# Kernel optimization log

Hardware: AMD Instinct MI355X
Metric: run time of the kernel (lower is better)

Reference implementation:

```python
import jax, jax.numpy as jnp
import numpy as np

N = 4_000_000
F = 8   # EXPERIMENTS['full'] feature count
H = 16  # hidden width of both MLPs
NBINS = 28


def _lin_init(k, i, o):
    return jax.random.normal(k, (i, o), jnp.float32) * (1.0 / np.sqrt(i))


def setup_inputs() -> dict:
    key = jax.random.key(0)
    ks = jax.random.split(key, 16)
    inp = {
        "x_feat": jax.random.normal(ks[0], (N, F), jnp.float32),
        # mh MLP params
        "mh_W1": _lin_init(ks[1], F, H), "mh_b1": jnp.zeros((H,), jnp.float32),
        "mh_W2": _lin_init(ks[2], H, H), "mh_b2": jnp.zeros((H,), jnp.float32),
        "mh_W3": _lin_init(ks[3], H, 1), "mh_b3": jnp.zeros((1,), jnp.float32),
        # mh_less MLP params (input dim 1 = Size)
        "ml_W1": _lin_init(ks[4], 1, H), "ml_b1": jnp.zeros((H,), jnp.float32),
        "ml_W2": _lin_init(ks[5], H, H), "ml_b2": jnp.zeros((H,), jnp.float32),
        "ml_W3": _lin_init(ks[6], H, 1), "ml_b3": jnp.zeros((1,), jnp.float32),
    }
    # deletion sizes in 1..40 (some > 28 exercise the skip branch)
    del_lens = jax.random.randint(ks[7], (N,), 1, 41, jnp.int32)
    eq = jax.random.bernoulli(ks[8], 0.3, (N,))
    alt = jax.random.randint(ks[9], (N,), 1, 41, jnp.int32)
    inp["del_lens"] = del_lens
    inp["mh_len"] = jnp.where(eq, del_lens, alt).astype(jnp.int32)
    return inp


def _mlp(x, W1, b1, W2, b2, W3, b3):
    h = jax.nn.sigmoid(x @ W1 + b1)
    h = jax.nn.sigmoid(h @ W2 + b2)
    return h @ W3 + b3  # [N, 1]


def reference(x_feat, mh_W1, mh_b1, mh_W2, mh_b2, mh_W3, mh_b3,
              ml_W1, ml_b1, ml_W2, ml_b2, ml_W3, ml_b3,
              del_lens, mh_len):
    dl_f = del_lens.astype(x_feat.dtype)[:, None]  # [N,1]
    # psi score: exp(phi - dl*0.25)
    mh_scores = jnp.exp(_mlp(x_feat, mh_W1, mh_b1, mh_W2, mh_b2, mh_W3, mh_b3)
                        - dl_f * 0.25)[:, 0]  # [N]
    # mh_less score on Size, added only where del_len == homologyLength
    mhless = jnp.exp(_mlp(dl_f, ml_W1, ml_b1, ml_W2, ml_b2, ml_W3, ml_b3)
                     - dl_f * 0.25)[:, 0]  # [N]
    mhfull_contribution = jnp.where(del_lens == mh_len, mhless, 0.0)
    y_mh_phi = mh_scores + mhfull_contribution  # [N]

    # mh_less scores for dl = 1..28
    dls = jnp.arange(1, NBINS + 1, dtype=x_feat.dtype)[:, None]  # [28,1]
    dl2_scores = jnp.exp(_mlp(dls, ml_W1, ml_b1, ml_W2, ml_b2, ml_W3, ml_b3)
                         - dls * 0.25)[:, 0]  # [28]

    # scatter-add mh_scores into bin (dl-1), skipping dl > 28
    vals = jnp.where(del_lens <= NBINS, mh_scores, 0.0)
    seg = jnp.clip(del_lens - 1, 0, NBINS - 1)
    mh_contribution = jax.ops.segment_sum(vals, seg, num_segments=NBINS)
    y_mh_less_phi = dl2_scores + mh_contribution  # [28]

    return (y_mh_phi, y_mh_less_phi)
```

## Files before the change

kernel.cpp:

```cpp
#include <hip/hip_runtime.h>
#include <math.h>

#define NBINS 28
#define L2E 1.44269504088896340736f

#define EXP2F(x) __builtin_amdgcn_exp2f(x)
#define RCPF(x)  __builtin_amdgcn_rcpf(x)

typedef __fp16 h2t __attribute__((ext_vector_type(2)));

static __device__ __forceinline__ float fdot2(h2t a, h2t b, float c) {
    return __builtin_amdgcn_fdot2(a, b, c, false);
}
static __device__ __forceinline__ h2t pkx(float lo, float hi) {
    return __builtin_amdgcn_cvt_pkrtz(lo, hi);
}
static __device__ __forceinline__ h2t asH2(float f) {
    union { float f; h2t h; } u; u.f = f; return u.h;
}

#define WS_TBL 0
#define WS_W1  64
#define WS_B1  192
#define WS_W2  208
#define WS_B2  464
#define WS_W3  480
#define WS_B3  496
#define WP_W1  512
#define WP_W2  576
#define WS_TOT 704

__global__ void prep_kernel(const float* __restrict__ mh_W1, const float* __restrict__ mh_b1,
                            const float* __restrict__ mh_W2, const float* __restrict__ mh_b2,
                            const float* __restrict__ mh_W3, const float* __restrict__ mh_b3,
                            const float* __restrict__ ml_W1, const float* __restrict__ ml_b1,
                            const float* __restrict__ ml_W2, const float* __restrict__ ml_b2,
                            const float* __restrict__ ml_W3, const float* __restrict__ ml_b3,
                            float* __restrict__ ws, float* __restrict__ out_bins) {
    const int t = threadIdx.x;
    for (int k = t; k < 128; k += 64) ws[WS_W1 + k] = -L2E * mh_W1[k];
    for (int k = t; k < 16;  k += 64) ws[WS_B1 + k] = -L2E * mh_b1[k];
    for (int k = t; k < 256; k += 64) ws[WS_W2 + k] = -L2E * mh_W2[k];
    for (int k = t; k < 16;  k += 64) ws[WS_B2 + k] = -L2E * mh_b2[k];
    for (int k = t; k < 16;  k += 64) ws[WS_W3 + k] =  L2E * mh_W3[k];
    if (t == 0) ws[WS_B3] = L2E * mh_b3[0];

    for (int k = t; k < 64; k += 64) {
        const int f2 = k >> 4, j = k & 15;
        union { __fp16 h[2]; float f; } u;
        u.h[0] = (__fp16)(-L2E * mh_W1[(2 * f2)     * 16 + j]);
        u.h[1] = (__fp16)(-L2E * mh_W1[(2 * f2 + 1) * 16 + j]);
        ws[WP_W1 + k] = u.f;
    }
    for (int k = t; k < 128; k += 64) {
        const int k2 = k >> 4, j = k & 15;
        union { __fp16 h[2]; float f; } u;
        u.h[0] = (__fp16)(-L2E * mh_W2[(2 * k2)     * 16 + j]);
        u.h[1] = (__fp16)(-L2E * mh_W2[(2 * k2 + 1) * 16 + j]);
        ws[WP_W2 + k] = u.f;
    }

    if (t < 40) {
        const float x = (float)(t + 1);
        float h1[16], h2[16];
        #pragma unroll
        for (int j = 0; j < 16; ++j)
            h1[j] = 1.0f / (1.0f + expf(-(x * ml_W1[j] + ml_b1[j])));
        #pragma unroll
        for (int j = 0; j < 16; ++j) {
            float a = ml_b2[j];
            #pragma unroll
            for (int k = 0; k < 16; ++k) a = fmaf(h1[k], ml_W2[k * 16 + j], a);
            h2[j] = 1.0f / (1.0f + expf(-a));
        }
        float phi = ml_b3[0];
        #pragma unroll
        for (int k = 0; k < 16; ++k) phi = fmaf(h2[k], ml_W3[k], phi);
        const float sc = expf(phi - 0.25f * x);
        ws[WS_TBL + t] = sc;
        if (t < NBINS) out_bins[t] = sc;
    }
}

__global__ __launch_bounds__(256) void main_kernel(
        const float4* __restrict__ x4,
        const int2* __restrict__ dl2p,
        const int2* __restrict__ ml2p,
        const float* __restrict__ ws,
        float2* __restrict__ out2,
        float* __restrict__ out_bins,
        int npair) {
    __shared__ float s_tbl[40];
    __shared__ float s_bins[4 * NBINS];
    const int tid = threadIdx.x;
    if (tid < 40) s_tbl[tid] = ws[WS_TBL + tid];
    if (tid < 4 * NBINS) s_bins[tid] = 0.0f;
    __syncthreads();

    const int p = blockIdx.x * 256 + tid;
    const bool active = (p < npair);
    const int pc = active ? p : 0;

    const float4 a0 = x4[4 * pc + 0];
    const float4 a1 = x4[4 * pc + 1];
    const float4 b0 = x4[4 * pc + 2];
    const float4 b1 = x4[4 * pc + 3];
    const int2 dl = dl2p[pc];
    const int2 ml = ml2p[pc];

    h2t xp0[4], xp1[4];
    xp0[0] = pkx(a0.x, a0.y); xp0[1] = pkx(a0.z, a0.w);
    xp0[2] = pkx(a1.x, a1.y); xp0[3] = pkx(a1.z, a1.w);
    xp1[0] = pkx(b0.x, b0.y); xp1[1] = pkx(b0.z, b0.w);
    xp1[2] = pkx(b1.x, b1.y); xp1[3] = pkx(b1.z, b1.w);

    float u0[16], u1[16];
    #pragma unroll
    for (int j = 0; j < 16; ++j) {
        const float b = ws[WS_B1 + j];
        u0[j] = b; u1[j] = b;
    }
    #pragma unroll
    for (int f2 = 0; f2 < 4; ++f2) {
        #pragma unroll
        for (int j = 0; j < 16; ++j) {
            const h2t w = asH2(ws[WP_W1 + f2 * 16 + j]);
            u0[j] = fdot2(xp0[f2], w, u0[j]);
            u1[j] = fdot2(xp1[f2], w, u1[j]);
        }
    }
    h2t hp0[8], hp1[8];
    #pragma unroll
    for (int k2 = 0; k2 < 8; ++k2) {
        const float h0a = RCPF(1.0f + EXP2F(u0[2 * k2]));
        const float h0b = RCPF(1.0f + EXP2F(u0[2 * k2 + 1]));
        const float h1a = RCPF(1.0f + EXP2F(u1[2 * k2]));
        const float h1b = RCPF(1.0f + EXP2F(u1[2 * k2 + 1]));
        hp0[k2] = pkx(h0a, h0b);
        hp1[k2] = pkx(h1a, h1b);
    }

    float v0[16], v1[16];
    #pragma unroll
    for (int j = 0; j < 16; ++j) {
        const float b = ws[WS_B2 + j];
        v0[j] = b; v1[j] = b;
    }
    #pragma unroll
    for (int k2 = 0; k2 < 8; ++k2) {
        #pragma unroll
        for (int j = 0; j < 16; ++j) {
            const h2t w = asH2(ws[WP_W2 + k2 * 16 + j]);
            v0[j] = fdot2(hp0[k2], w, v0[j]);
            v1[j] = fdot2(hp1[k2], w, v1[j]);
        }
    }

    float phi0 = ws[WS_B3], phi1 = phi0;
    #pragma unroll
    for (int j = 0; j < 16; ++j) {
        const float w3 = ws[WS_W3 + j];
        phi0 = fmaf(RCPF(1.0f + EXP2F(v0[j])), w3, phi0);
        phi1 = fmaf(RCPF(1.0f + EXP2F(v1[j])), w3, phi1);
    }
    const float sc0 = EXP2F(fmaf((float)dl.x, -0.25f * L2E, phi0));
    const float sc1 = EXP2F(fmaf((float)dl.y, -0.25f * L2E, phi1));

    if (active) {
        const int i0 = min(max(dl.x, 1), 40) - 1;
        const int i1 = min(max(dl.y, 1), 40) - 1;
        const float add0 = (dl.x == ml.x) ? s_tbl[i0] : 0.0f;
        const float add1 = (dl.y == ml.y) ? s_tbl[i1] : 0.0f;
        out2[p] = make_float2(sc0 + add0, sc1 + add1);
        float* myb = &s_bins[(tid >> 6) * NBINS];
        if (dl.x >= 1 && dl.x <= NBINS) unsafeAtomicAdd(&myb[dl.x - 1], sc0);
        if (dl.y >= 1 && dl.y <= NBINS) unsafeAtomicAdd(&myb[dl.y - 1], sc1);
    }

    __syncthreads();
    if (tid < NBINS) {
        const float bsum = s_bins[tid] + s_bins[NBINS + tid] +
                           s_bins[2 * NBINS + tid] + s_bins[3 * NBINS + tid];
        unsafeAtomicAdd(&out_bins[tid], bsum);
    }
}

extern "C" void kernel_launch(void* const* d_in, const int* in_sizes, int n_in,
                              void* d_out, int out_size, void* d_ws, size_t ws_size,
                              hipStream_t stream) {
    const int n = in_sizes[0] / 8;

    const float* x_feat = (const float*)d_in[0];
    const float* mh_W1  = (const float*)d_in[1];
    const float* mh_b1  = (const float*)d_in[2];
    const float* mh_W2  = (const float*)d_in[3];
    const float* mh_b2  = (const float*)d_in[4];
    const float* mh_W3  = (const float*)d_in[5];
    const float* mh_b3  = (const float*)d_in[6];
    const float* ml_W1  = (const float*)d_in[7];
    const float* ml_b1  = (const float*)d_in[8];
    const float* ml_W2  = (const float*)d_in[9];
    const float* ml_b2  = (const float*)d_in[10];
    const float* ml_W3  = (const float*)d_in[11];
    const float* ml_b3  = (const float*)d_in[12];
    const int* del_lens = (const int*)d_in[13];
    const int* mh_len   = (const int*)d_in[14];

    float* out      = (float*)d_out;
    float* out_bins = out + n;
    float* ws       = (float*)d_ws;

    prep_kernel<<<dim3(1), dim3(64), 0, stream>>>(
        mh_W1, mh_b1, mh_W2, mh_b2, mh_W3, mh_b3,
        ml_W1, ml_b1, ml_W2, ml_b2, ml_W3, ml_b3,
        ws, out_bins);

    const int npair = n / 2;
    const int nblocks = (npair + 255) / 256;
    main_kernel<<<dim3(nblocks), dim3(256), 0, stream>>>(
        (const float4*)x_feat, (const int2*)del_lens, (const int2*)mh_len,
        ws, (float2*)out, out_bins, npair);
}
```

Measured before the change: 311.6 us.

## Use grid-stride persistent blocks with register prefetch of next pair

Replaces the one-pair-per-thread launch with a fixed grid of up to 2048 blocks that loop over pairs in a grid stride. Each iteration loads the next pair's features and indices into registers before computing the current one, so memory latency overlaps with the MLP arithmetic. It also cuts the number of per-block shared-bin flushes and global atomics on the bin outputs. The cost is higher register pressure from the prefetched data, which may lower occupancy.

```diff
diff --git a/kernel.cpp b/kernel.cpp
--- a/kernel.cpp
+++ b/kernel.cpp
@@ -82,6 +82,11 @@
     }
 }
 
+struct PairIn {
+    float4 a0, a1, b0, b1;
+    int2 dl, ml;
+};
+
 __global__ __launch_bounds__(256) void main_kernel(
         const float4* __restrict__ x4,
         const int2* __restrict__ dl2p,
@@ -89,7 +94,7 @@
         const float* __restrict__ ws,
         float2* __restrict__ out2,
         float* __restrict__ out_bins,
-        int npair) {
+        int npair, int stride, int iters) {
     __shared__ float s_tbl[40];
     __shared__ float s_bins[4 * NBINS];
     const int tid = threadIdx.x;
@@ -97,84 +102,103 @@
     if (tid < 4 * NBINS) s_bins[tid] = 0.0f;
     __syncthreads();
 
-    const int p = blockIdx.x * 256 + tid;
-    const bool active = (p < npair);
-    const int pc = active ? p : 0;
-
-    const float4 a0 = x4[4 * pc + 0];
-    const float4 a1 = x4[4 * pc + 1];
-    const float4 b0 = x4[4 * pc + 2];
-    const float4 b1 = x4[4 * pc + 3];
-    const int2 dl = dl2p[pc];
-    const int2 ml = ml2p[pc];
-
-    h2t xp0[4], xp1[4];
-    xp0[0] = pkx(a0.x, a0.y); xp0[1] = pkx(a0.z, a0.w);
-    xp0[2] = pkx(a1.x, a1.y); xp0[3] = pkx(a1.z, a1.w);
-    xp1[0] = pkx(b0.x, b0.y); xp1[1] = pkx(b0.z, b0.w);
-    xp1[2] = pkx(b1.x, b1.y); xp1[3] = pkx(b1.z, b1.w);
-
-    float u0[16], u1[16];
-    #pragma unroll
-    for (int j = 0; j < 16; ++j) {
-        const float b = ws[WS_B1 + j];
-        u0[j] = b; u1[j] = b;
-    }
-    #pragma unroll
-    for (int f2 = 0; f2 < 4; ++f2) {
-        #pragma unroll
-        for (int j = 0; j < 16; ++j) {
-            const h2t w = asH2(ws[WP_W1 + f2 * 16 + j]);
-            u0[j] = fdot2(xp0[f2], w, u0[j]);
-            u1[j] = fdot2(xp1[f2], w, u1[j]);
-        }
-    }
-    h2t hp0[8], hp1[8];
-    #pragma unroll
-    for (int k2 = 0; k2 < 8; ++k2) {
-        const float h0a = RCPF(1.0f + EXP2F(u0[2 * k2]));
-        const float h0b = RCPF(1.0f + EXP2F(u0[2 * k2 + 1]));
-        const float h1a = RCPF(1.0f + EXP2F(u1[2 * k2]));
-        const float h1b = RCPF(1.0f + EXP2F(u1[2 * k2 + 1]));
-        hp0[k2] = pkx(h0a, h0b);
-        hp1[k2] = pkx(h1a, h1b);
-    }
-
-    float v0[16], v1[16];
-    #pragma unroll
-    for (int j = 0; j < 16; ++j) {
-        const float b = ws[WS_B2 + j];
-        v0[j] = b; v1[j] = b;
-    }
-    #pragma unroll
-    for (int k2 = 0; k2 < 8; ++k2) {
-        #pragma unroll
-        for (int j = 0; j < 16; ++j) {
-            const h2t w = asH2(ws[WP_W2 + k2 * 16 + j]);
-            v0[j] = fdot2(hp0[k2], w, v0[j]);
-            v1[j] = fdot2(hp1[k2], w, v1[j]);
-        }
-    }
-
-    float phi0 = ws[WS_B3], phi1 = phi0;
-    #pragma unroll
-    for (int j = 0; j < 16; ++j) {
-        const float w3 = ws[WS_W3 + j];
-        phi0 = fmaf(RCPF(1.0f + EXP2F(v0[j])), w3, phi0);
-        phi1 = fmaf(RCPF(1.0f + EXP2F(v1[j])), w3, phi1);
-    }
-    const float sc0 = EXP2F(fmaf((float)dl.x, -0.25f * L2E, phi0));
-    const float sc1 = EXP2F(fmaf((float)dl.y, -0.25f * L2E, phi1));
-
-    if (active) {
-        const int i0 = min(max(dl.x, 1), 40) - 1;
-        const int i1 = min(max(dl.y, 1), 40) - 1;
-        const float add0 = (dl.x == ml.x) ? s_tbl[i0] : 0.0f;
-        const float add1 = (dl.y == ml.y) ? s_tbl[i1] : 0.0f;
-        out2[p] = make_float2(sc0 + add0, sc1 + add1);
-        float* myb = &s_bins[(tid >> 6) * NBINS];
-        if (dl.x >= 1 && dl.x <= NBINS) unsafeAtomicAdd(&myb[dl.x - 1], sc0);
-        if (dl.y >= 1 && dl.y <= NBINS) unsafeAtomicAdd(&myb[dl.y - 1], sc1);
+    float* myb = &s_bins[(tid >> 6) * NBINS];
+
+    int p = blockIdx.x * 256 + tid;
+
+    PairIn cur;
+    {
+        const int pc = (p < npair) ? p : 0;
+        cur.a0 = x4[4 * pc + 0]; cur.a1 = x4[4 * pc + 1];
+        cur.b0 = x4[4 * pc + 2]; cur.b1 = x4[4 * pc + 3];
+        cur.dl = dl2p[pc];       cur.ml = ml2p[pc];
+    }
+
+    #pragma unroll 1
+    for (int it = 0; it < iters; ++it) {
+        PairIn nxt;
+        const int pn = p + stride;
+        if (it + 1 < iters) {
+            const int pcn = (pn < npair) ? pn : 0;
+            nxt.a0 = x4[4 * pcn + 0]; nxt.a1 = x4[4 * pcn + 1];
+            nxt.b0 = x4[4 * pcn + 2]; nxt.b1 = x4[4 * pcn + 3];
+            nxt.dl = dl2p[pcn];       nxt.ml = ml2p[pcn];
+        }
+
+        const bool active = (p < npair);
+        const int2 dl = cur.dl;
+        const int2 ml = cur.ml;
+
+        h2t xp0[4], xp1[4];
+        xp0[0] = pkx(cur.a0.x, cur.a0.y); xp0[1] = pkx(cur.a0.z, cur.a0.w);
+        xp0[2] = pkx(cur.a1.x, cur.a1.y); xp0[3] = pkx(cur.a1.z, cur.a1.w);
+        xp1[0] = pkx(cur.b0.x, cur.b0.y); xp1[1] = pkx(cur.b0.z, cur.b0.w);
+        xp1[2] = pkx(cur.b1.x, cur.b1.y); xp1[3] = pkx(cur.b1.z, cur.b1.w);
+
+        float u0[16], u1[16];
+        #pragma unroll
+        for (int j = 0; j < 16; ++j) {
+            const float b = ws[WS_B1 + j];
+            u0[j] = b; u1[j] = b;
+        }
+        #pragma unroll
+        for (int f2 = 0; f2 < 4; ++f2) {
+            #pragma unroll
+            for (int j = 0; j < 16; ++j) {
+                const h2t w = asH2(ws[WP_W1 + f2 * 16 + j]);
+                u0[j] = fdot2(xp0[f2], w, u0[j]);
+                u1[j] = fdot2(xp1[f2], w, u1[j]);
+            }
+        }
+        h2t hp0[8], hp1[8];
+        #pragma unroll
+        for (int k2 = 0; k2 < 8; ++k2) {
+            const float h0a = RCPF(1.0f + EXP2F(u0[2 * k2]));
+            const float h0b = RCPF(1.0f + EXP2F(u0[2 * k2 + 1]));
+            const float h1a = RCPF(1.0f + EXP2F(u1[2 * k2]));
+            const float h1b = RCPF(1.0f + EXP2F(u1[2 * k2 + 1]));
+            hp0[k2] = pkx(h0a, h0b);
+            hp1[k2] = pkx(h1a, h1b);
+        }
+
+        float v0[16], v1[16];
+        #pragma unroll
+        for (int j = 0; j < 16; ++j) {
+            const float b = ws[WS_B2 + j];
+            v0[j] = b; v1[j] = b;
+        }
+        #pragma unroll
+        for (int k2 = 0; k2 < 8; ++k2) {
+            #pragma unroll
+            for (int j = 0; j < 16; ++j) {
+                const h2t w = asH2(ws[WP_W2 + k2 * 16 + j]);
+                v0[j] = fdot2(hp0[k2], w, v0[j]);
+                v1[j] = fdot2(hp1[k2], w, v1[j]);
+            }
+        }
+
+        float phi0 = ws[WS_B3], phi1 = phi0;
+        #pragma unroll
+        for (int j = 0; j < 16; ++j) {
+            const float w3 = ws[WS_W3 + j];
+            phi0 = fmaf(RCPF(1.0f + EXP2F(v0[j])), w3, phi0);
+            phi1 = fmaf(RCPF(1.0f + EXP2F(v1[j])), w3, phi1);
+        }
+        const float sc0 = EXP2F(fmaf((float)dl.x, -0.25f * L2E, phi0));
+        const float sc1 = EXP2F(fmaf((float)dl.y, -0.25f * L2E, phi1));
+
+        if (active) {
+            const int i0 = min(max(dl.x, 1), 40) - 1;
+            const int i1 = min(max(dl.y, 1), 40) - 1;
+            const float add0 = (dl.x == ml.x) ? s_tbl[i0] : 0.0f;
+            const float add1 = (dl.y == ml.y) ? s_tbl[i1] : 0.0f;
+            out2[p] = make_float2(sc0 + add0, sc1 + add1);
+            if (dl.x >= 1 && dl.x <= NBINS) unsafeAtomicAdd(&myb[dl.x - 1], sc0);
+            if (dl.y >= 1 && dl.y <= NBINS) unsafeAtomicAdd(&myb[dl.y - 1], sc1);
+        }
+
+        cur = nxt;
+        p = pn;
     }
 
     __syncthreads();
@@ -216,8 +240,12 @@
         ws, out_bins);
 
     const int npair = n / 2;
-    const int nblocks = (npair + 255) / 256;
+    int nblocks = 2048;
+    const int needed = (npair + 255) / 256;
+    if (needed < nblocks) nblocks = needed;
+    const int stride = nblocks * 256;
+    const int iters = (npair + stride - 1) / stride;
     main_kernel<<<dim3(nblocks), dim3(256), 0, stream>>>(
         (const float4*)x_feat, (const int2*)del_lens, (const int2*)mh_len,
-        ws, (float2*)out, out_bins, npair);
-}
+        ws, (float2*)out, out_bins, npair, stride, iters);
+}
```

New measurement: 267.4 us. 14.2% less time.
